# Kernel optimization log

Hardware: AMD Instinct MI355X
Metric: run time of the kernel (lower is better)

Reference implementation:

```python
import jax, jax.numpy as jnp
import numpy as np


def _gcn_conv(X, src, dst, norm, W, n_nodes):
    # gather + normalized aggregate (SpMM) then dense linear (GEMM)
    msg = X[src] * norm[:, None]                       # [E, F]
    agg = jax.ops.segment_sum(msg, dst, num_segments=n_nodes)  # [N, F]
    return agg @ W                                     # [N, F_out]


def setup_inputs() -> dict:
    key = jax.random.key(0)
    k1, k2, k3, k4, k5 = jax.random.split(key, 5)
    N, E, D_IN, D_HID, D_OUT = 50000, 800000, 128, 128, 64
    X = jax.random.normal(k1, (N, D_IN), dtype=jnp.float32)
    edge_index = jax.random.randint(k2, (2, E), 0, N, dtype=jnp.int64)
    s = 1.0 / np.sqrt(D_IN)
    W1 = jax.random.normal(k3, (D_IN, D_HID), dtype=jnp.float32) * s
    W2 = jax.random.normal(k4, (D_HID, D_HID), dtype=jnp.float32) * s
    W3 = jax.random.normal(k5, (D_HID, D_OUT), dtype=jnp.float32) * s
    return {"X": X, "edge_index": edge_index, "W1": W1, "W2": W2, "W3": W3}


def reference(X, edge_index, W1, W2, W3):
    n_nodes = X.shape[0]
    src, dst = edge_index[0], edge_index[1]
    # symmetric degree normalization D^-1/2 A D^-1/2 (degrees from edge list)
    ones = jnp.ones(src.shape[0], dtype=X.dtype)
    deg = jax.ops.segment_sum(ones, dst, num_segments=n_nodes)
    deg = jnp.maximum(deg, 1.0)
    dinv = jax.lax.rsqrt(deg)
    norm = dinv[src] * dinv[dst]                       # [E]
    h = jax.nn.relu(_gcn_conv(X, src, dst, norm, W1, n_nodes))
    h = jax.nn.relu(_gcn_conv(h, src, dst, norm, W2, n_nodes))
    h = jax.nn.relu(_gcn_conv(h, src, dst, norm, W3, n_nodes))
    return jax.nn.softmax(h, axis=-1)
```

## Files before the change

### kernel.cpp

```cpp
#include <hip/hip_runtime.h>
#include <hip/hip_bf16.h>

typedef __attribute__((ext_vector_type(8))) short short8;
typedef __attribute__((ext_vector_type(4))) short short4v;
typedef __attribute__((ext_vector_type(4))) float f32x4;

static inline size_t ws_align(size_t x) { return (x + 511) & ~((size_t)511); }

static __device__ inline unsigned short f2bf(float f) {
    __hip_bfloat16 h = __float2bfloat16(f);
    return __builtin_bit_cast(unsigned short, h);
}

__global__ void sniff_kernel(const unsigned short* __restrict__ w1,
                             const unsigned int* __restrict__ ei,
                             int* __restrict__ flags) {
    int i = threadIdx.x;
    unsigned e = (w1[2 * i] >> 7) & 0xFF;
    unsigned long long m1 = __ballot(e >= 100 && e <= 130);
    unsigned long long m2 = __ballot(ei[2 * i + 1] == 0u);
    if (i == 0) {
        flags[0] = (__popcll(m1) < 48) ? 1 : 0;
        flags[1] = (__popcll(m2) >= 48) ? 1 : 0;
    }
}

__global__ void hist_kernel(const int* __restrict__ ei, const int* __restrict__ flags,
                            int* __restrict__ counts, int* __restrict__ loff, int E) {
    int e = blockIdx.x * blockDim.x + threadIdx.x;
    if (e < E) {
        int d = flags[1] ? ei[2 * (size_t)E + 2 * e] : ei[(size_t)E + e];
        loff[e] = atomicAdd(&counts[d], 1);
    }
}

__global__ __launch_bounds__(256) void alloc_kernel(const int* __restrict__ counts,
                                                    float* __restrict__ dinv,
                                                    int* __restrict__ rowptr,
                                                    int* __restrict__ total, int N) {
    int n = blockIdx.x * blockDim.x + threadIdx.x;
    int lane = threadIdx.x & 63;
    int c = (n < N) ? counts[n] : 0;
    if (n < N) {
        int d = (c < 1) ? 1 : c;
        dinv[n] = rsqrtf((float)d);
    }
    int incl = c;
#pragma unroll
    for (int off = 1; off < 64; off <<= 1) {
        int v = __shfl_up(incl, off, 64);
        if (lane >= off) incl += v;
    }
    int wavetot = __shfl(incl, 63, 64);
    int base = 0;
    if (lane == 0) base = atomicAdd(total, wavetot);
    base = __shfl(base, 0, 64);
    if (n < N) rowptr[n] = base + incl - c;
}

__global__ void fill_kernel(const int* __restrict__ ei, const int* __restrict__ flags,
                            const float* __restrict__ dinv, const int* __restrict__ rowptr,
                            const int* __restrict__ loff, int2* __restrict__ edgedat, int E) {
    int e = blockIdx.x * blockDim.x + threadIdx.x;
    if (e < E) {
        int s, d;
        if (flags[1]) {
            s = ei[2 * e];
            d = ei[2 * (size_t)E + 2 * e];
        } else {
            s = ei[e];
            d = ei[(size_t)E + e];
        }
        int pos = rowptr[d] + loff[e];
        float wt = dinv[s] * dinv[d];
        edgedat[pos] = make_int2(s, __float_as_int(wt));
    }
}


template <int FOUT>
__global__ __launch_bounds__(256) void gemm_kernel(const void* __restrict__ Araw, int a_follows,
                                                   const void* __restrict__ Wraw,
                                                   const int* __restrict__ flags,
                                                   unsigned short* __restrict__ out, int Nrows) {
    constexpr int K = 128;
    constexpr int NT = FOUT / 16;
    constexpr int LDB = K + 8;
    __shared__ __align__(16) unsigned short bt[FOUT * LDB];

    const int tid = threadIdx.x;
    const int in_fp32 = flags[0];
    const int a_fp32 = a_follows & in_fp32;

    constexpr int TOT4 = K * FOUT / 4;
    if (in_fp32) {
        const float* Wf = (const float*)Wraw;
        for (int i = tid; i < TOT4; i += 256) {
            int idx = i * 4;
            int k = idx / FOUT;
            int n = idx & (FOUT - 1);
            float4 v = *(const float4*)(const void*)(Wf + idx);
            bt[(n + 0) * LDB + k] = f2bf(v.x);
            bt[(n + 1) * LDB + k] = f2bf(v.y);
            bt[(n + 2) * LDB + k] = f2bf(v.z);
            bt[(n + 3) * LDB + k] = f2bf(v.w);
        }
    } else {
        const unsigned short* Ws = (const unsigned short*)Wraw;
        for (int i = tid; i < TOT4; i += 256) {
            int idx = i * 4;
            int k = idx / FOUT;
            int n = idx & (FOUT - 1);
            short4v v = *(const short4v*)(const void*)(Ws + idx);
#pragma unroll
            for (int j = 0; j < 4; j++) bt[(n + j) * LDB + k] = ((const unsigned short*)&v)[j];
        }
    }

    const int wave = tid >> 6;
    const int lane = tid & 63;
    const int quad = lane >> 4;
    const int r16 = lane & 15;

    short8 afrag[2][4];
#pragma unroll
    for (int t = 0; t < 2; t++) {
        int arow = blockIdx.x * 128 + t * 64 + wave * 16 + r16;
        if (arow > Nrows - 1) arow = Nrows - 1;
        if (a_fp32) {
            const float* Ap = (const float*)Araw + (size_t)arow * K + quad * 8;
#pragma unroll
            for (int kk = 0; kk < 4; kk++) {
                float4 f0 = *(const float4*)(const void*)(Ap + kk * 32);
                float4 f1 = *(const float4*)(const void*)(Ap + kk * 32 + 4);
                short8 r;
                r[0] = (short)f2bf(f0.x); r[1] = (short)f2bf(f0.y);
                r[2] = (short)f2bf(f0.z); r[3] = (short)f2bf(f0.w);
                r[4] = (short)f2bf(f1.x); r[5] = (short)f2bf(f1.y);
                r[6] = (short)f2bf(f1.z); r[7] = (short)f2bf(f1.w);
                afrag[t][kk] = r;
            }
        } else {
            const unsigned short* Ap = (const unsigned short*)Araw + (size_t)arow * K + quad * 8;
#pragma unroll
            for (int kk = 0; kk < 4; kk++) afrag[t][kk] = *(const short8*)(const void*)(Ap + kk * 32);
        }
    }

    __syncthreads();

    f32x4 acc[2][NT];
#pragma unroll
    for (int t = 0; t < 2; t++)
#pragma unroll
        for (int nt = 0; nt < NT; nt++) acc[t][nt] = (f32x4){0.f, 0.f, 0.f, 0.f};

#pragma unroll
    for (int kk = 0; kk < 4; kk++) {
#pragma unroll
        for (int nt = 0; nt < NT; nt++) {
            short8 b = *(const short8*)(const void*)(&bt[(nt * 16 + r16) * LDB + kk * 32 + quad * 8]);
#pragma unroll
            for (int t = 0; t < 2; t++)
                acc[t][nt] = __builtin_amdgcn_mfma_f32_16x16x32_bf16(afrag[t][kk], b, acc[t][nt], 0, 0, 0);
        }
    }

#pragma unroll
    for (int t = 0; t < 2; t++) {
#pragma unroll
        for (int nt = 0; nt < NT; nt++) {
#pragma unroll
            for (int r = 0; r < 4; r++) {
                float v = acc[t][nt][r];
                float o = __shfl_xor(v, 1, 64);
                int row = blockIdx.x * 128 + t * 64 + wave * 16 + quad * 4 + r;
                if (((lane & 1) == 0) && row < Nrows) {
                    __hip_bfloat162 pk;
                    pk.x = __float2bfloat16(v);
                    pk.y = __float2bfloat16(o);
                    *(__hip_bfloat162*)(out + (size_t)row * FOUT + nt * 16 + r16) = pk;
                }
            }
        }
    }
}


__global__ __launch_bounds__(256) void spmm128_kernel(const int2* __restrict__ edgedat,
                                                      const int* __restrict__ rowptr,
                                                      const int* __restrict__ counts,
                                                      const __hip_bfloat162* __restrict__ Hin,
                                                      __hip_bfloat162* __restrict__ Hout, int N) {
    int wid = (blockIdx.x * 256 + threadIdx.x) >> 6;
    if (wid >= N) return;
    int lane = threadIdx.x & 63;
    int n = __builtin_amdgcn_readfirstlane(wid);
    int start = __builtin_amdgcn_readfirstlane(rowptr[n]);
    int len = __builtin_amdgcn_readfirstlane(counts[n]);
    float ax = 0.f, ay = 0.f;
    int j = 0;
    for (; j + 8 <= len; j += 8) {
        int2 ed[8];
        __hip_bfloat162 hv[8];
#pragma unroll
        for (int u = 0; u < 8; u++) ed[u] = edgedat[start + j + u];
#pragma unroll
        for (int u = 0; u < 8; u++) hv[u] = Hin[(size_t)ed[u].x * 64 + lane];
#pragma unroll
        for (int u = 0; u < 8; u++) {
            float w = __int_as_float(ed[u].y);
            ax += w * __bfloat162float(hv[u].x);
            ay += w * __bfloat162float(hv[u].y);
        }
    }
    for (; j + 4 <= len; j += 4) {
        int2 ed[4];
        __hip_bfloat162 hv[4];
#pragma unroll
        for (int u = 0; u < 4; u++) ed[u] = edgedat[start + j + u];
#pragma unroll
        for (int u = 0; u < 4; u++) hv[u] = Hin[(size_t)ed[u].x * 64 + lane];
#pragma unroll
        for (int u = 0; u < 4; u++) {
            float w = __int_as_float(ed[u].y);
            ax += w * __bfloat162float(hv[u].x);
            ay += w * __bfloat162float(hv[u].y);
        }
    }
    for (; j < len; j++) {
        int2 ed = edgedat[start + j];
        float wt = __int_as_float(ed.y);
        __hip_bfloat162 hv = Hin[(size_t)ed.x * 64 + lane];
        ax += wt * __bfloat162float(hv.x);
        ay += wt * __bfloat162float(hv.y);
    }
    __hip_bfloat162 pk;
    pk.x = __float2bfloat16(fmaxf(ax, 0.f));
    pk.y = __float2bfloat16(fmaxf(ay, 0.f));
    Hout[(size_t)n * 64 + lane] = pk;
}

__global__ __launch_bounds__(256) void spmm64_softmax_kernel(const int2* __restrict__ edgedat,
                                                             const int* __restrict__ rowptr,
                                                             const int* __restrict__ counts,
                                                             const __hip_bfloat16* __restrict__ Hin,
                                                             const int* __restrict__ flags,
                                                             void* __restrict__ Out, int N) {
    int wid = (blockIdx.x * 256 + threadIdx.x) >> 6;
    if (wid >= N) return;
    int lane = threadIdx.x & 63;
    int n = __builtin_amdgcn_readfirstlane(wid);
    int start = __builtin_amdgcn_readfirstlane(rowptr[n]);
    int len = __builtin_amdgcn_readfirstlane(counts[n]);
    float a = 0.f;
    int j = 0;
    for (; j + 8 <= len; j += 8) {
        int2 ed[8];
        float hv[8];
#pragma unroll
        for (int u = 0; u < 8; u++) ed[u] = edgedat[start + j + u];
#pragma unroll
        for (int u = 0; u < 8; u++) hv[u] = __bfloat162float(Hin[(size_t)ed[u].x * 64 + lane]);
#pragma unroll
        for (int u = 0; u < 8; u++) a += __int_as_float(ed[u].y) * hv[u];
    }
    for (; j + 4 <= len; j += 4) {
        int2 ed[4];
        float hv[4];
#pragma unroll
        for (int u = 0; u < 4; u++) ed[u] = edgedat[start + j + u];
#pragma unroll
        for (int u = 0; u < 4; u++) hv[u] = __bfloat162float(Hin[(size_t)ed[u].x * 64 + lane]);
#pragma unroll
        for (int u = 0; u < 4; u++) a += __int_as_float(ed[u].y) * hv[u];
    }
    for (; j < len; j++) {
        int2 ed = edgedat[start + j];
        a += __int_as_float(ed.y) * __bfloat162float(Hin[(size_t)ed.x * 64 + lane]);
    }
    a = fmaxf(a, 0.f);
    float m = a;
#pragma unroll
    for (int off = 32; off > 0; off >>= 1) m = fmaxf(m, __shfl_xor(m, off, 64));
    float e = __expf(a - m);
    float s = e;
#pragma unroll
    for (int off = 32; off > 0; off >>= 1) s += __shfl_xor(s, off, 64);
    float r = e / s;
    if (flags[0]) {
        ((float*)Out)[(size_t)n * 64 + lane] = r;
    } else {
        ((unsigned short*)Out)[(size_t)n * 64 + lane] = f2bf(r);
    }
}


extern "C" void kernel_launch(void* const* d_in, const int* in_sizes, int n_in,
                              void* d_out, int out_size, void* d_ws, size_t ws_size,
                              hipStream_t stream) {
    const void* X  = d_in[0];
    const int*  ei = (const int*)d_in[1];
    const void* W1 = d_in[2];
    const void* W2 = d_in[3];
    const void* W3 = d_in[4];

    const int N = in_sizes[0] / 128;
    const int E = in_sizes[1] / 2;

    char* ws = (char*)d_ws;
    size_t off = 0;
    int* counts = (int*)(ws + off);   off += ws_align((size_t)N * 4);
    int* total  = (int*)(ws + off);   off += ws_align(64);
    const size_t zero_bytes = off;
    int* flags    = (int*)(ws + off);   off += ws_align(64);
    int* rowptr   = (int*)(ws + off);   off += ws_align((size_t)N * 4);
    float* dinv   = (float*)(ws + off); off += ws_align((size_t)N * 4);
    int* loff     = (int*)(ws + off);   off += ws_align((size_t)E * 4);
    int2* edgedat = (int2*)(ws + off);  off += ws_align((size_t)E * 8);
    unsigned short* HA = (unsigned short*)(ws + off); off += ws_align((size_t)N * 128 * 2);
    unsigned short* HB = (unsigned short*)(ws + off); off += ws_align((size_t)N * 128 * 2);

    hipMemsetAsync(d_ws, 0, zero_bytes, stream);

    sniff_kernel<<<1, 64, 0, stream>>>((const unsigned short*)W1, (const unsigned int*)ei, flags);
    hist_kernel<<<(E + 255) / 256, 256, 0, stream>>>(ei, flags, counts, loff, E);
    alloc_kernel<<<(N + 255) / 256, 256, 0, stream>>>(counts, dinv, rowptr, total, N);
    fill_kernel<<<(E + 255) / 256, 256, 0, stream>>>(ei, flags, dinv, rowptr, loff, edgedat, E);

    const int gblocks = (N + 127) / 128;
    const int sblocks = (N * 64 + 255) / 256;

    gemm_kernel<128><<<gblocks, 256, 0, stream>>>(X, 1, W1, flags, HA, N);
    spmm128_kernel<<<sblocks, 256, 0, stream>>>(edgedat, rowptr, counts,
                                                (const __hip_bfloat162*)HA, (__hip_bfloat162*)HB, N);
    gemm_kernel<128><<<gblocks, 256, 0, stream>>>(HB, 0, W2, flags, HA, N);
    spmm128_kernel<<<sblocks, 256, 0, stream>>>(edgedat, rowptr, counts,
                                                (const __hip_bfloat162*)HA, (__hip_bfloat162*)HB, N);
    gemm_kernel<64><<<gblocks, 256, 0, stream>>>(HB, 0, W3, flags, HA, N);
    spmm64_softmax_kernel<<<sblocks, 256, 0, stream>>>(edgedat, rowptr, counts,
                                                       (const __hip_bfloat16*)HA, flags, d_out, N);
}
```

Baseline: 271.5 us.

## Process two nodes per wavefront in SpMM and inline dtype sniffing

After: 288.2 us. +6.2%, slower.

```diff
diff --git a/kernel.cpp b/kernel.cpp
--- a/kernel.cpp
+++ b/kernel.cpp
@@ -11,32 +11,36 @@
     __hip_bfloat16 h = __float2bfloat16(f);
     return __builtin_bit_cast(unsigned short, h);
 }
-
-__global__ void sniff_kernel(const unsigned short* __restrict__ w1,
-                             const unsigned int* __restrict__ ei,
-                             int* __restrict__ flags) {
-    int i = threadIdx.x;
+static __device__ inline float bfbits2f(unsigned short u) {
+    unsigned x = ((unsigned)u) << 16;
+    return __builtin_bit_cast(float, x);
+}
+
+static __device__ inline int sniff_fp32(const unsigned short* __restrict__ w1) {
+    int i = threadIdx.x & 63;
     unsigned e = (w1[2 * i] >> 7) & 0xFF;
-    unsigned long long m1 = __ballot(e >= 100 && e <= 130);
-    unsigned long long m2 = __ballot(ei[2 * i + 1] == 0u);
-    if (i == 0) {
-        flags[0] = (__popcll(m1) < 48) ? 1 : 0;
-        flags[1] = (__popcll(m2) >= 48) ? 1 : 0;
-    }
-}
-
-__global__ void hist_kernel(const int* __restrict__ ei, const int* __restrict__ flags,
+    unsigned long long m = __ballot(e >= 100 && e <= 130);
+    return (__popcll(m) < 48) ? 1 : 0;
+}
+static __device__ inline int sniff_is64(const unsigned int* __restrict__ ei) {
+    int i = threadIdx.x & 63;
+    unsigned long long m = __ballot(ei[2 * i + 1] == 0u);
+    return (__popcll(m) >= 48) ? 1 : 0;
+}
+
+__global__ void hist_kernel(const int* __restrict__ ei,
                             int* __restrict__ counts, int* __restrict__ loff, int E) {
+    int is64 = sniff_is64((const unsigned int*)ei);
     int e = blockIdx.x * blockDim.x + threadIdx.x;
     if (e < E) {
-        int d = flags[1] ? ei[2 * (size_t)E + 2 * e] : ei[(size_t)E + e];
+        int d = is64 ? ei[2 * (size_t)E + 2 * e] : ei[(size_t)E + e];
         loff[e] = atomicAdd(&counts[d], 1);
     }
 }
 
 __global__ __launch_bounds__(256) void alloc_kernel(const int* __restrict__ counts,
                                                     float* __restrict__ dinv,
-                                                    int* __restrict__ rowptr,
+                                                    int2* __restrict__ rc,
                                                     int* __restrict__ total, int N) {
     int n = blockIdx.x * blockDim.x + threadIdx.x;
     int lane = threadIdx.x & 63;
@@ -55,23 +59,24 @@
     int base = 0;
     if (lane == 0) base = atomicAdd(total, wavetot);
     base = __shfl(base, 0, 64);
-    if (n < N) rowptr[n] = base + incl - c;
-}
-
-__global__ void fill_kernel(const int* __restrict__ ei, const int* __restrict__ flags,
-                            const float* __restrict__ dinv, const int* __restrict__ rowptr,
+    if (n < N) rc[n] = make_int2(base + incl - c, c);
+}
+
+__global__ void fill_kernel(const int* __restrict__ ei,
+                            const float* __restrict__ dinv, const int2* __restrict__ rc,
                             const int* __restrict__ loff, int2* __restrict__ edgedat, int E) {
+    int is64 = sniff_is64((const unsigned int*)ei);
     int e = blockIdx.x * blockDim.x + threadIdx.x;
     if (e < E) {
         int s, d;
-        if (flags[1]) {
+        if (is64) {
             s = ei[2 * e];
             d = ei[2 * (size_t)E + 2 * e];
         } else {
             s = ei[e];
             d = ei[(size_t)E + e];
         }
-        int pos = rowptr[d] + loff[e];
+        int pos = rc[d].x + loff[e];
         float wt = dinv[s] * dinv[d];
         edgedat[pos] = make_int2(s, __float_as_int(wt));
     }
@@ -81,7 +86,7 @@
 template <int FOUT>
 __global__ __launch_bounds__(256) void gemm_kernel(const void* __restrict__ Araw, int a_follows,
                                                    const void* __restrict__ Wraw,
-                                                   const int* __restrict__ flags,
+                                                   const unsigned short* __restrict__ w1sniff,
                                                    unsigned short* __restrict__ out, int Nrows) {
     constexpr int K = 128;
     constexpr int NT = FOUT / 16;
@@ -89,7 +94,7 @@
     __shared__ __align__(16) unsigned short bt[FOUT * LDB];
 
     const int tid = threadIdx.x;
-    const int in_fp32 = flags[0];
+    const int in_fp32 = sniff_fp32(w1sniff);
     const int a_fp32 = a_follows & in_fp32;
 
     constexpr int TOT4 = K * FOUT / 4;
@@ -188,110 +193,113 @@
 
 
 __global__ __launch_bounds__(256) void spmm128_kernel(const int2* __restrict__ edgedat,
-                                                      const int* __restrict__ rowptr,
-                                                      const int* __restrict__ counts,
-                                                      const __hip_bfloat162* __restrict__ Hin,
-                                                      __hip_bfloat162* __restrict__ Hout, int N) {
+                                                      const int2* __restrict__ rc,
+                                                      const unsigned short* __restrict__ Hin,
+                                                      unsigned short* __restrict__ Hout, int N) {
     int wid = (blockIdx.x * 256 + threadIdx.x) >> 6;
-    if (wid >= N) return;
     int lane = threadIdx.x & 63;
-    int n = __builtin_amdgcn_readfirstlane(wid);
-    int start = __builtin_amdgcn_readfirstlane(rowptr[n]);
-    int len = __builtin_amdgcn_readfirstlane(counts[n]);
-    float ax = 0.f, ay = 0.f;
-    int j = 0;
-    for (; j + 8 <= len; j += 8) {
+    int half = lane >> 5;
+    int li = lane & 31;
+    int n = wid * 2 + half;
+    int nc = (n < N) ? n : (N - 1);
+    int2 r_ = rc[nc];
+    int start = r_.x;
+    int len = (n < N) ? r_.y : 0;
+    int maxlen = max(len, __shfl_xor(len, 32, 64));
+
+    float a0 = 0.f, a1 = 0.f, a2 = 0.f, a3 = 0.f;
+    for (int j = 0; j < maxlen; j += 8) {
         int2 ed[8];
-        __hip_bfloat162 hv[8];
-#pragma unroll
-        for (int u = 0; u < 8; u++) ed[u] = edgedat[start + j + u];
-#pragma unroll
-        for (int u = 0; u < 8; u++) hv[u] = Hin[(size_t)ed[u].x * 64 + lane];
-#pragma unroll
-        for (int u = 0; u < 8; u++) {
-            float w = __int_as_float(ed[u].y);
-            ax += w * __bfloat162float(hv[u].x);
-            ay += w * __bfloat162float(hv[u].y);
-        }
-    }
-    for (; j + 4 <= len; j += 4) {
-        int2 ed[4];
-        __hip_bfloat162 hv[4];
-#pragma unroll
-        for (int u = 0; u < 4; u++) ed[u] = edgedat[start + j + u];
-#pragma unroll
-        for (int u = 0; u < 4; u++) hv[u] = Hin[(size_t)ed[u].x * 64 + lane];
-#pragma unroll
-        for (int u = 0; u < 4; u++) {
-            float w = __int_as_float(ed[u].y);
-            ax += w * __bfloat162float(hv[u].x);
-            ay += w * __bfloat162float(hv[u].y);
-        }
-    }
-    for (; j < len; j++) {
-        int2 ed = edgedat[start + j];
-        float wt = __int_as_float(ed.y);
-        __hip_bfloat162 hv = Hin[(size_t)ed.x * 64 + lane];
-        ax += wt * __bfloat162float(hv.x);
-        ay += wt * __bfloat162float(hv.y);
-    }
-    __hip_bfloat162 pk;
-    pk.x = __float2bfloat16(fmaxf(ax, 0.f));
-    pk.y = __float2bfloat16(fmaxf(ay, 0.f));
-    Hout[(size_t)n * 64 + lane] = pk;
+#pragma unroll
+        for (int u = 0; u < 8; u++) {
+            int jj = j + u;
+            int idx = (jj < len) ? (start + jj) : start;
+            ed[u] = edgedat[idx];
+        }
+        short4v hv[8];
+#pragma unroll
+        for (int u = 0; u < 8; u++) {
+            int s = ed[u].x;
+            s = (s < 0) ? 0 : ((s > N - 1) ? (N - 1) : s);
+            hv[u] = *(const short4v*)(const void*)(Hin + (size_t)s * 128 + li * 4);
+        }
+#pragma unroll
+        for (int u = 0; u < 8; u++) {
+            float w = ((j + u) < len) ? __int_as_float(ed[u].y) : 0.f;
+            a0 += w * bfbits2f((unsigned short)hv[u][0]);
+            a1 += w * bfbits2f((unsigned short)hv[u][1]);
+            a2 += w * bfbits2f((unsigned short)hv[u][2]);
+            a3 += w * bfbits2f((unsigned short)hv[u][3]);
+        }
+    }
+    if (n < N) {
+        short4v o;
+        o[0] = (short)f2bf(fmaxf(a0, 0.f));
+        o[1] = (short)f2bf(fmaxf(a1, 0.f));
+        o[2] = (short)f2bf(fmaxf(a2, 0.f));
+        o[3] = (short)f2bf(fmaxf(a3, 0.f));
+        *(short4v*)(Hout + (size_t)n * 128 + li * 4) = o;
+    }
 }
 
 __global__ __launch_bounds__(256) void spmm64_softmax_kernel(const int2* __restrict__ edgedat,
-                                                             const int* __restrict__ rowptr,
-                                                             const int* __restrict__ counts,
-                                                             const __hip_bfloat16* __restrict__ Hin,
-                                                             const int* __restrict__ flags,
+                                                             const int2* __restrict__ rc,
+                                                             const unsigned short* __restrict__ Hin,
+                                                             const unsigned short* __restrict__ w1sniff,
                                                              void* __restrict__ Out, int N) {
+    int out_fp32 = sniff_fp32(w1sniff);
     int wid = (blockIdx.x * 256 + threadIdx.x) >> 6;
-    if (wid >= N) return;
     int lane = threadIdx.x & 63;
-    int n = __builtin_amdgcn_readfirstlane(wid);
-    int start = __builtin_amdgcn_readfirstlane(rowptr[n]);
-    int len = __builtin_amdgcn_readfirstlane(counts[n]);
-    float a = 0.f;
-    int j = 0;
-    for (; j + 8 <= len; j += 8) {
+    int half = lane >> 5;
+    int li = lane & 31;
+    int n = wid * 2 + half;
+    int nc = (n < N) ? n : (N - 1);
+    int2 r_ = rc[nc];
+    int start = r_.x;
+    int len = (n < N) ? r_.y : 0;
+    int maxlen = max(len, __shfl_xor(len, 32, 64));
+
+    float a0 = 0.f, a1 = 0.f;
+    for (int j = 0; j < maxlen; j += 8) {
         int2 ed[8];
-        float hv[8];
-#pragma unroll
-        for (int u = 0; u < 8; u++) ed[u] = edgedat[start + j + u];
-#pragma unroll
-        for (int u = 0; u < 8; u++) hv[u] = __bfloat162float(Hin[(size_t)ed[u].x * 64 + lane]);
-#pragma unroll
-        for (int u = 0; u < 8; u++) a += __int_as_float(ed[u].y) * hv[u];
-    }
-    for (; j + 4 <= len; j += 4) {
-        int2 ed[4];
-        float hv[4];
-#pragma unroll
-        for (int u = 0; u < 4; u++) ed[u] = edgedat[start + j + u];
-#pragma unroll
-        for (int u = 0; u < 4; u++) hv[u] = __bfloat162float(Hin[(size_t)ed[u].x * 64 + lane]);
-#pragma unroll
-        for (int u = 0; u < 4; u++) a += __int_as_float(ed[u].y) * hv[u];
-    }
-    for (; j < len; j++) {
-        int2 ed = edgedat[start + j];
-        a += __int_as_float(ed.y) * __bfloat162float(Hin[(size_t)ed.x * 64 + lane]);
-    }
-    a = fmaxf(a, 0.f);
-    float m = a;
-#pragma unroll
-    for (int off = 32; off > 0; off >>= 1) m = fmaxf(m, __shfl_xor(m, off, 64));
-    float e = __expf(a - m);
-    float s = e;
-#pragma unroll
-    for (int off = 32; off > 0; off >>= 1) s += __shfl_xor(s, off, 64);
-    float r = e / s;
-    if (flags[0]) {
-        ((float*)Out)[(size_t)n * 64 + lane] = r;
-    } else {
-        ((unsigned short*)Out)[(size_t)n * 64 + lane] = f2bf(r);
+#pragma unroll
+        for (int u = 0; u < 8; u++) {
+            int jj = j + u;
+            int idx = (jj < len) ? (start + jj) : start;
+            ed[u] = edgedat[idx];
+        }
+        unsigned hv[8];
+#pragma unroll
+        for (int u = 0; u < 8; u++) {
+            int s = ed[u].x;
+            s = (s < 0) ? 0 : ((s > N - 1) ? (N - 1) : s);
+            hv[u] = *(const unsigned*)(const void*)(Hin + (size_t)s * 64 + li * 2);
+        }
+#pragma unroll
+        for (int u = 0; u < 8; u++) {
+            float w = ((j + u) < len) ? __int_as_float(ed[u].y) : 0.f;
+            a0 += w * bfbits2f((unsigned short)(hv[u] & 0xFFFF));
+            a1 += w * bfbits2f((unsigned short)(hv[u] >> 16));
+        }
+    }
+    a0 = fmaxf(a0, 0.f);
+    a1 = fmaxf(a1, 0.f);
+    float m = fmaxf(a0, a1);
+#pragma unroll
+    for (int off = 16; off > 0; off >>= 1) m = fmaxf(m, __shfl_xor(m, off, 64));
+    float e0 = __expf(a0 - m), e1 = __expf(a1 - m);
+    float s = e0 + e1;
+#pragma unroll
+    for (int off = 16; off > 0; off >>= 1) s += __shfl_xor(s, off, 64);
+    float r0 = e0 / s, r1 = e1 / s;
+    if (n < N) {
+        if (out_fp32) {
+            float2 pk = make_float2(r0, r1);
+            *(float2*)((float*)Out + (size_t)n * 64 + li * 2) = pk;
+        } else {
+            unsigned pk = (unsigned)f2bf(r0) | ((unsigned)f2bf(r1) << 16);
+            *(unsigned*)((unsigned short*)Out + (size_t)n * 64 + li * 2) = pk;
+        }
     }
 }
 
@@ -304,6 +312,7 @@
     const void* W1 = d_in[2];
     const void* W2 = d_in[3];
     const void* W3 = d_in[4];
+    const unsigned short* W1s = (const unsigned short*)W1;
 
     const int N = in_sizes[0] / 128;
     const int E = in_sizes[1] / 2;
@@ -313,31 +322,27 @@
     int* counts = (int*)(ws + off);   off += ws_align((size_t)N * 4);
     int* total  = (int*)(ws + off);   off += ws_align(64);
     const size_t zero_bytes = off;
-    int* flags    = (int*)(ws + off);   off += ws_align(64);
-    int* rowptr   = (int*)(ws + off);   off += ws_align((size_t)N * 4);
+    int2* rc      = (int2*)(ws + off);  off += ws_align((size_t)N * 8);
     float* dinv   = (float*)(ws + off); off += ws_align((size_t)N * 4);
     int* loff     = (int*)(ws + off);   off += ws_align((size_t)E * 4);
-    int2* edgedat = (int2*)(ws + off);  off += ws_align((size_t)E * 8);
+    int2* edgedat = (int2*)(ws + off);  off += ws_align((size_t)(E + 64) * 8);
     unsigned short* HA = (unsigned short*)(ws + off); off += ws_align((size_t)N * 128 * 2);
     unsigned short* HB = (unsigned short*)(ws + off); off += ws_align((size_t)N * 128 * 2);
 
     hipMemsetAsync(d_ws, 0, zero_bytes, stream);
 
-    sniff_kernel<<<1, 64, 0, stream>>>((const unsigned short*)W1, (const unsigned int*)ei, flags);
-    hist_kernel<<<(E + 255) / 256, 256, 0, stream>>>(ei, flags, counts, loff, E);
-    alloc_kernel<<<(N + 255) / 256, 256, 0, stream>>>(counts, dinv, rowptr, total, N);
-    fill_kernel<<<(E + 255) / 256, 256, 0, stream>>>(ei, flags, dinv, rowptr, loff, edgedat, E);
+    hist_kernel<<<(E + 255) / 256, 256, 0, stream>>>(ei, counts, loff, E);
+    alloc_kernel<<<(N + 255) / 256, 256, 0, stream>>>(counts, dinv, rc, total, N);
+    fill_kernel<<<(E + 255) / 256, 256, 0, stream>>>(ei, dinv, rc, loff, edgedat, E);
 
     const int gblocks = (N + 127) / 128;
-    const int sblocks = (N * 64 + 255) / 256;
-
-    gemm_kernel<128><<<gblocks, 256, 0, stream>>>(X, 1, W1, flags, HA, N);
-    spmm128_kernel<<<sblocks, 256, 0, stream>>>(edgedat, rowptr, counts,
-                                                (const __hip_bfloat162*)HA, (__hip_bfloat162*)HB, N);
-    gemm_kernel<128><<<gblocks, 256, 0, stream>>>(HB, 0, W2, flags, HA, N);
-    spmm128_kernel<<<sblocks, 256, 0, stream>>>(edgedat, rowptr, counts,
-                                                (const __hip_bfloat162*)HA, (__hip_bfloat162*)HB, N);
-    gemm_kernel<64><<<gblocks, 256, 0, stream>>>(HB, 0, W3, flags, HA, N);
-    spmm64_softmax_kernel<<<sblocks, 256, 0, stream>>>(edgedat, rowptr, counts,
-                                                       (const __hip_bfloat16*)HA, flags, d_out, N);
-}
+    const int waves2 = (N + 1) / 2;
+    const int sblocks = (waves2 * 64 + 255) / 256;
+
+    gemm_kernel<128><<<gblocks, 256, 0, stream>>>(X, 1, W1, W1s, HA, N);
+    spmm128_kernel<<<sblocks, 256, 0, stream>>>(edgedat, rc, HA, HB, N);
+    gemm_kernel<128><<<gblocks, 256, 0, stream>>>(HB, 0, W2, W1s, HA, N);
+    spmm128_kernel<<<sblocks, 256, 0, stream>>>(edgedat, rc, HA, HB, N);
+    gemm_kernel<64><<<gblocks, 256, 0, stream>>>(HB, 0, W3, W1s, HA, N);
+    spmm64_softmax_kernel<<<sblocks, 256, 0, stream>>>(edgedat, rc, HA, W1s, d_out, N);
+}
```
